# Optimization experiments

Measured on AMD Instinct MI355X. Metric: run time of the kernel, lower is better.

## Reference

```python
import jax, jax.numpy as jnp
import numpy as np

B, S, D, H = 2, 2048, 1024, 16
HD = D // H  # head_dim = 64


def setup_inputs() -> dict:
    key = jax.random.key(0)
    ks = jax.random.split(key, 11)
    s = 0.02  # keep projections well-scaled
    return {
        "Q": jax.random.normal(ks[0], (B, S, D), jnp.float32),
        "K": jax.random.normal(ks[1], (B, S, D), jnp.float32),
        "V": jax.random.normal(ks[2], (B, S, D), jnp.float32),
        "Wq": jax.random.normal(ks[3], (D, D), jnp.float32) * s,
        "bq": jax.random.normal(ks[4], (D,), jnp.float32) * s,
        "Wk": jax.random.normal(ks[5], (D, D), jnp.float32) * s,
        "bk": jax.random.normal(ks[6], (D,), jnp.float32) * s,
        "Wv": jax.random.normal(ks[7], (D, D), jnp.float32) * s,
        "bv": jax.random.normal(ks[8], (D,), jnp.float32) * s,
        "Wo": jax.random.normal(ks[9], (D, D), jnp.float32) * s,
        "bo": jax.random.normal(ks[10], (D,), jnp.float32) * s,
    }


def reference(Q, K, V, Wq, bq, Wk, bk, Wv, bv, Wo, bo):
    b, s, d = Q.shape
    # projections (torch Linear: x @ W.T + b)
    q = (Q @ Wq.T + bq).reshape(b, s, H, HD).transpose(0, 2, 1, 3)  # [B,H,S,HD]
    k = (K @ Wk.T + bk).reshape(b, s, H, HD).transpose(0, 2, 1, 3)
    v = (V @ Wv.T + bv).reshape(b, s, H, HD).transpose(0, 2, 1, 3)
    # scaled dot-product scores: [B,H,S,S]
    scale = 1.0 / jnp.sqrt(jnp.asarray(HD, q.dtype))
    scores = jnp.einsum("bhqd,bhkd->bhqk", q, k) * scale
    # module's explicit max-subtract before softmax
    scores = scores - jnp.max(scores, axis=-1, keepdims=True)
    attn = jax.nn.softmax(scores, axis=-1)
    # dropout p=0.0 (eval) -> identity; renormalize-after-dropout kept verbatim
    attn = attn / jnp.sum(attn, axis=-1, keepdims=True)
    ctx = jnp.einsum("bhqk,bhkd->bhqd", attn, v)  # [B,H,S,HD]
    ctx = ctx.transpose(0, 2, 1, 3).reshape(b, s, d)
    out = ctx @ Wo.T + bo
    return out
```

## Files before the change

kernel.cpp:

```cpp
#include <hip/hip_runtime.h>

#define SS 2048
#define SD 1024
#define SH 16
#define SHD 64
#define MROWS 4096
#define LOG2E 1.44269504088896340736f

typedef __attribute__((ext_vector_type(8))) short short8;
typedef __attribute__((ext_vector_type(4))) short short4v;
typedef __attribute__((ext_vector_type(4))) float floatx4;
typedef __attribute__((ext_vector_type(4))) unsigned short ushort4v;
typedef unsigned short u16;
typedef unsigned int u32;

#define AS1 __attribute__((address_space(1)))
#define AS3 __attribute__((address_space(3)))

__device__ inline u16 f2bf(float v) {
  u32 x = __builtin_bit_cast(u32, v);
  x = x + 0x7fffu + ((x >> 16) & 1u);
  return (u16)(x >> 16);
}

__global__ __launch_bounds__(256) void cast_all(
    const float* __restrict__ q, const float* __restrict__ k,
    const float* __restrict__ v, const float* __restrict__ wq,
    const float* __restrict__ wk, const float* __restrict__ wv,
    const float* __restrict__ wo, u16* __restrict__ out) {
  int i = blockIdx.x * 256 + threadIdx.x;
  const float* src;
  int idx;
  if (i < 3145728) {
    int a = i >> 20;
    src = (a == 0) ? q : ((a == 1) ? k : v);
    idx = i & 1048575;
  } else {
    int j = i - 3145728;
    int a = j >> 18;
    src = (a == 0) ? wq : ((a == 1) ? wk : ((a == 2) ? wv : wo));
    idx = j & 262143;
  }
  float4 f = ((const float4*)src)[idx];
  ushort4v o;
  o[0] = f2bf(f.x); o[1] = f2bf(f.y); o[2] = f2bf(f.z); o[3] = f2bf(f.w);
  ((ushort4v*)out)[i] = o;
}

__global__ __launch_bounds__(256) void gemm_bt(
    const u16* __restrict__ Aall, const u16* __restrict__ Wall,
    const float* __restrict__ b0, const float* __restrict__ b1,
    const float* __restrict__ b2, u16* __restrict__ outb,
    float* __restrict__ outf, int mode, float qscale) {
  __shared__ u16 lds_a[128 * 32];
  __shared__ u16 lds_w[128 * 32];
  int z = blockIdx.z;
  const u16* A = Aall + (size_t)z * (MROWS * (size_t)SD);
  const u16* W = Wall + (size_t)z * (SD * (size_t)SD);
  const float* bias = (z == 0) ? b0 : ((z == 1) ? b1 : b2);
  float scale = (mode == 0 && z == 0) ? qscale : 1.0f;

  int tid = threadIdx.x;
  int lane = tid & 63, wave = tid >> 6;
  int l16 = lane & 15, quad = lane >> 4;
  int wm = (wave >> 1) * 64, wn = (wave & 1) * 64;
  int tm = blockIdx.y * 128, tn = blockIdx.x * 128;

  floatx4 acc[4][4];
  floatx4 zf = {0.f, 0.f, 0.f, 0.f};
#pragma unroll
  for (int r = 0; r < 4; r++)
#pragma unroll
    for (int c = 0; c < 4; c++) acc[r][c] = zf;

  int srow = wave * 16 + (lane >> 2);
  int scol8 = (lane & 3) * 8;
  const u16* pa0 = A + (size_t)(tm + srow) * SD + scol8;
  const u16* pa1 = pa0 + (size_t)64 * SD;
  const u16* pw0 = W + (size_t)(tn + srow) * SD + scol8;
  const u16* pw1 = pw0 + (size_t)64 * SD;
  AS3 u16* la0 = (AS3 u16*)&lds_a[wave * 512];
  AS3 u16* la1 = (AS3 u16*)&lds_a[(wave + 4) * 512];
  AS3 u16* lw0 = (AS3 u16*)&lds_w[wave * 512];
  AS3 u16* lw1 = (AS3 u16*)&lds_w[(wave + 4) * 512];

  for (int k0 = 0; k0 < SD; k0 += 32) {
    __builtin_amdgcn_global_load_lds((const AS1 void*)pa0, (AS3 void*)la0, 16, 0, 0);
    __builtin_amdgcn_global_load_lds((const AS1 void*)pa1, (AS3 void*)la1, 16, 0, 0);
    __builtin_amdgcn_global_load_lds((const AS1 void*)pw0, (AS3 void*)lw0, 16, 0, 0);
    __builtin_amdgcn_global_load_lds((const AS1 void*)pw1, (AS3 void*)lw1, 16, 0, 0);
    pa0 += 32; pa1 += 32; pw0 += 32; pw1 += 32;
    __syncthreads();
    short8 af[4], wf[4];
#pragma unroll
    for (int r = 0; r < 4; r++)
      af[r] = *(short8*)&lds_a[(wm + r * 16 + l16) * 32 + quad * 8];
#pragma unroll
    for (int c = 0; c < 4; c++)
      wf[c] = *(short8*)&lds_w[(wn + c * 16 + l16) * 32 + quad * 8];
#pragma unroll
    for (int r = 0; r < 4; r++)
#pragma unroll
      for (int c = 0; c < 4; c++)
        acc[r][c] = __builtin_amdgcn_mfma_f32_16x16x32_bf16(af[r], wf[c], acc[r][c], 0, 0, 0);
    __syncthreads();
  }

  if (mode == 0) {
    u16* ob = outb + (size_t)z * (MROWS * (size_t)SD);
    if (z < 2) {
#pragma unroll
      for (int r = 0; r < 4; r++) {
#pragma unroll
        for (int c = 0; c < 4; c++) {
          int gn = tn + wn + c * 16 + l16;
          float bv = bias[gn];
          int h = gn >> 6, hd = gn & 63;
#pragma unroll
          for (int g = 0; g < 4; g++) {
            int gm = tm + wm + r * 16 + quad * 4 + g;
            int bb = gm >> 11, ss = gm & 2047;
            float val = (acc[r][c][g] + bv) * scale;
            ob[(size_t)(((bb * SH + h) * SS + ss) * SHD + hd)] = f2bf(val);
          }
        }
      }
    } else {
      int h = (tn + wn) >> 6;
      int bb = (tm + wm) >> 11;
      int kt = ((tm + wm) & 2047) >> 6;
      u16* vbase = ob + (size_t)(bb * SH + h) * (SS * SHD) + (size_t)kt * 4096 +
                   (l16 * 4 + quad) * 8;
#pragma unroll
      for (int c = 0; c < 4; c++) {
        int gn = tn + wn + c * 16 + l16;
        float bv = bias[gn];
#pragma unroll
        for (int rp = 0; rp < 2; rp++) {
          union { u16 u[8]; short8 s; } pk;
#pragma unroll
          for (int g = 0; g < 4; g++) {
            pk.u[g]     = f2bf(acc[2 * rp][c][g] + bv);
            pk.u[4 + g] = f2bf(acc[2 * rp + 1][c][g] + bv);
          }
          *(short8*)&vbase[(c * 2 + rp) * 512] = pk.s;
        }
      }
    }
  } else {
#pragma unroll
    for (int r = 0; r < 4; r++) {
#pragma unroll
      for (int c = 0; c < 4; c++) {
        int gn = tn + wn + c * 16 + l16;
        float bv = bias[gn];
#pragma unroll
        for (int g = 0; g < 4; g++) {
          int gm = tm + wm + r * 16 + quad * 4 + g;
          outf[(size_t)gm * SD + gn] = acc[r][c][g] + bv;
        }
      }
    }
  }
}

__global__ __launch_bounds__(128, 2) void attn(
    const u16* __restrict__ qb, const u16* __restrict__ kb,
    const u16* __restrict__ vfrag, u16* __restrict__ ctxb) {
  int lane = threadIdx.x & 63;
  int wave = threadIdx.x >> 6;
  int l16 = lane & 15, quad = lane >> 4;

  int raw = blockIdx.x;
  int xcd = raw & 7, slot = raw >> 3;
  int bh = xcd + 8 * (slot >> 5);
  int qt = slot & 31;
  int b = bh >> 4, h = bh & 15;
  int base = bh * (SS * SHD);
  int q0 = qt * 64;

  const u16* kp = kb + base + l16 * 64 + quad * 8;
  const u16* vp = vfrag + base + (l16 * 4 + quad) * 8;

  short8 qf[4][2];
#pragma unroll
  for (int t = 0; t < 4; t++)
#pragma unroll
    for (int hh = 0; hh < 2; hh++)
      qf[t][hh] = *(const short8*)&qb[base + (q0 + t * 16 + l16) * SHD + hh * 32 + quad * 8];

  floatx4 zf = {0.f, 0.f, 0.f, 0.f};
  floatx4 acc[4][4], accl[4];
#pragma unroll
  for (int t = 0; t < 4; t++) {
    accl[t] = zf;
#pragma unroll
    for (int c = 0; c < 4; c++) acc[t][c] = zf;
  }
  const short8 ones8 = {0x3F80, 0x3F80, 0x3F80, 0x3F80,
                        0x3F80, 0x3F80, 0x3F80, 0x3F80};

  int ktbase = wave * 16;
  short8 kf[4][2], vf[4][2];
  {
    const u16* p = kp + ktbase * 4096;
#pragma unroll
    for (int ct = 0; ct < 4; ct++)
#pragma unroll
      for (int hh = 0; hh < 2; hh++)
        kf[ct][hh] = *(const short8*)&p[ct * 1024 + hh * 32];
    const u16* pv = vp + ktbase * 4096;
#pragma unroll
    for (int c = 0; c < 4; c++)
#pragma unroll
      for (int c2 = 0; c2 < 2; c2++)
        vf[c][c2] = *(const short8*)&pv[(c * 2 + c2) * 512];
  }

#pragma unroll 1
  for (int i = 0; i < 16; i++) {
    int nt = ktbase + ((i + 1) & 15);
    const u16* kpn = kp + nt * 4096;
    const u16* vpn = vp + nt * 4096;
#pragma unroll
    for (int c2 = 0; c2 < 2; c2++) {
      const int ct0 = 2 * c2, ct1 = 2 * c2 + 1;
      floatx4 se[4], so[4];
#pragma unroll
      for (int t = 0; t < 4; t++) {
        floatx4 zz = zf;
        zz = __builtin_amdgcn_mfma_f32_16x16x32_bf16(kf[ct0][0], qf[t][0], zz, 0, 0, 0);
        zz = __builtin_amdgcn_mfma_f32_16x16x32_bf16(kf[ct0][1], qf[t][1], zz, 0, 0, 0);
        se[t] = zz;
        floatx4 ww = zf;
        ww = __builtin_amdgcn_mfma_f32_16x16x32_bf16(kf[ct1][0], qf[t][0], ww, 0, 0, 0);
        ww = __builtin_amdgcn_mfma_f32_16x16x32_bf16(kf[ct1][1], qf[t][1], ww, 0, 0, 0);
        so[t] = ww;
      }
      kf[ct0][0] = *(const short8*)&kpn[ct0 * 1024];
      kf[ct0][1] = *(const short8*)&kpn[ct0 * 1024 + 32];
      kf[ct1][0] = *(const short8*)&kpn[ct1 * 1024];
      kf[ct1][1] = *(const short8*)&kpn[ct1 * 1024 + 32];
#pragma unroll
      for (int t = 0; t < 4; t++) {
        u32 e0 = __builtin_bit_cast(u32, __builtin_amdgcn_exp2f(se[t][0]));
        u32 e1 = __builtin_bit_cast(u32, __builtin_amdgcn_exp2f(se[t][1]));
        u32 e2 = __builtin_bit_cast(u32, __builtin_amdgcn_exp2f(se[t][2]));
        u32 e3 = __builtin_bit_cast(u32, __builtin_amdgcn_exp2f(se[t][3]));
        u32 o0 = __builtin_bit_cast(u32, __builtin_amdgcn_exp2f(so[t][0]));
        u32 o1 = __builtin_bit_cast(u32, __builtin_amdgcn_exp2f(so[t][1]));
        u32 o2 = __builtin_bit_cast(u32, __builtin_amdgcn_exp2f(so[t][2]));
        u32 o3 = __builtin_bit_cast(u32, __builtin_amdgcn_exp2f(so[t][3]));
        union { u32 u[4]; short8 s; } pa;
        pa.u[0] = __builtin_amdgcn_perm(e1, e0, 0x07060302);
        pa.u[1] = __builtin_amdgcn_perm(e3, e2, 0x07060302);
        pa.u[2] = __builtin_amdgcn_perm(o1, o0, 0x07060302);
        pa.u[3] = __builtin_amdgcn_perm(o3, o2, 0x07060302);
#pragma unroll
        for (int c = 0; c < 4; c++)
          acc[t][c] = __builtin_amdgcn_mfma_f32_16x16x32_bf16(pa.s, vf[c][c2], acc[t][c], 0, 0, 0);
        accl[t] = __builtin_amdgcn_mfma_f32_16x16x32_bf16(pa.s, ones8, accl[t], 0, 0, 0);
      }
#pragma unroll
      for (int c = 0; c < 4; c++)
        vf[c][c2] = *(const short8*)&vpn[(c * 2 + c2) * 512];
    }
  }

  __shared__ floatx4 red[2][64][11];
  int ow = 1 - wave;
#pragma unroll
  for (int t = 0; t < 4; t++) {
    if ((t >> 1) == ow) {
#pragma unroll
      for (int c = 0; c < 4; c++) red[ow][lane][(t & 1) * 5 + c] = acc[t][c];
      red[ow][lane][(t & 1) * 5 + 4] = accl[t];
    }
  }
  __syncthreads();
#pragma unroll
  for (int t = 0; t < 4; t++) {
    if ((t >> 1) == wave) {
#pragma unroll
      for (int c = 0; c < 4; c++) acc[t][c] += red[wave][lane][(t & 1) * 5 + c];
      accl[t] += red[wave][lane][(t & 1) * 5 + 4];
    }
  }

#pragma unroll
  for (int t = 0; t < 4; t++) {
    if ((t >> 1) == wave) {
#pragma unroll
      for (int g = 0; g < 4; g++) {
        float invg = 1.0f / accl[t][g];
        int qrow = q0 + t * 16 + quad * 4 + g;
#pragma unroll
        for (int c = 0; c < 4; c++) {
          int hd = c * 16 + l16;
          ctxb[(size_t)((b * SS + qrow) * SD + h * SHD + hd)] = f2bf(acc[t][c][g] * invg);
        }
      }
    }
  }
}

extern "C" void kernel_launch(void* const* d_in, const int* in_sizes, int n_in,
                              void* d_out, int out_size, void* d_ws, size_t ws_size,
                              hipStream_t stream) {
  const float* Q  = (const float*)d_in[0];
  const float* Kp = (const float*)d_in[1];
  const float* Vp = (const float*)d_in[2];
  const float* Wq = (const float*)d_in[3];
  const float* bq = (const float*)d_in[4];
  const float* Wk = (const float*)d_in[5];
  const float* bk = (const float*)d_in[6];
  const float* Wv = (const float*)d_in[7];
  const float* bv = (const float*)d_in[8];
  const float* Wo = (const float*)d_in[9];
  const float* bo = (const float*)d_in[10];

  u16* xb   = (u16*)d_ws;
  u16* wb   = xb + (size_t)3 * 4194304;
  u16* qkvb = wb + (size_t)4 * 1048576;
  u16* ctxb = qkvb + (size_t)3 * 4194304;
  float* out = (float*)d_out;

  cast_all<<<dim3(16384), dim3(256), 0, stream>>>(Q, Kp, Vp, Wq, Wk, Wv, Wo, xb);

  const float qscale = 0.125f * LOG2E;
  gemm_bt<<<dim3(8, 32, 3), dim3(256), 0, stream>>>(
      xb, wb, bq, bk, bv, qkvb, (float*)nullptr, 0, qscale);

  attn<<<dim3(1024), dim3(128), 0, stream>>>(
      qkvb, qkvb + (size_t)4194304, qkvb + (size_t)2 * 4194304, ctxb);

  gemm_bt<<<dim3(8, 32, 1), dim3(256), 0, stream>>>(
      ctxb, wb + (size_t)3 * 1048576, bo, bo, bo,
      (u16*)nullptr, out, 1, 1.0f);
}
```

Measured before the change: 242.6 us.

## Use swizzled 64-wide K tiles in GEMM and fragment-packed Q/K layout

The projection GEMM now stages 64-wide K slices per iteration in an XOR-swizzled LDS layout, halving the number of barriers and reducing bank conflicts. It also sets an occupancy hint of three blocks per SM. For Q and K, the epilogue stages the tile through LDS and writes MFMA-fragment-ordered chunks, so each lane does one contiguous 16-byte load in the attention kernel instead of strided row loads. The cost is twice the LDS per block and an extra LDS round trip plus a barrier in the epilogue.

```diff
diff --git a/kernel.cpp b/kernel.cpp
--- a/kernel.cpp
+++ b/kernel.cpp
@@ -47,13 +47,14 @@
   ((ushort4v*)out)[i] = o;
 }
 
-__global__ __launch_bounds__(256) void gemm_bt(
+__global__ __launch_bounds__(256, 3) void gemm_bt(
     const u16* __restrict__ Aall, const u16* __restrict__ Wall,
     const float* __restrict__ b0, const float* __restrict__ b1,
     const float* __restrict__ b2, u16* __restrict__ outb,
     float* __restrict__ outf, int mode, float qscale) {
-  __shared__ u16 lds_a[128 * 32];
-  __shared__ u16 lds_w[128 * 32];
+  __shared__ u16 smem[16384];
+  u16* lds_a = smem;
+  u16* lds_w = smem + 8192;
   int z = blockIdx.z;
   const u16* A = Aall + (size_t)z * (MROWS * (size_t)SD);
   const u16* W = Wall + (size_t)z * (SD * (size_t)SD);
@@ -73,57 +74,81 @@
 #pragma unroll
     for (int c = 0; c < 4; c++) acc[r][c] = zf;
 
-  int srow = wave * 16 + (lane >> 2);
-  int scol8 = (lane & 3) * 8;
-  const u16* pa0 = A + (size_t)(tm + srow) * SD + scol8;
-  const u16* pa1 = pa0 + (size_t)64 * SD;
-  const u16* pw0 = W + (size_t)(tn + srow) * SD + scol8;
-  const u16* pw1 = pw0 + (size_t)64 * SD;
-  AS3 u16* la0 = (AS3 u16*)&lds_a[wave * 512];
-  AS3 u16* la1 = (AS3 u16*)&lds_a[(wave + 4) * 512];
-  AS3 u16* lw0 = (AS3 u16*)&lds_w[wave * 512];
-  AS3 u16* lw1 = (AS3 u16*)&lds_w[(wave + 4) * 512];
-
-  for (int k0 = 0; k0 < SD; k0 += 32) {
-    __builtin_amdgcn_global_load_lds((const AS1 void*)pa0, (AS3 void*)la0, 16, 0, 0);
-    __builtin_amdgcn_global_load_lds((const AS1 void*)pa1, (AS3 void*)la1, 16, 0, 0);
-    __builtin_amdgcn_global_load_lds((const AS1 void*)pw0, (AS3 void*)lw0, 16, 0, 0);
-    __builtin_amdgcn_global_load_lds((const AS1 void*)pw1, (AS3 void*)lw1, 16, 0, 0);
-    pa0 += 32; pa1 += 32; pw0 += 32; pw1 += 32;
+  const u16* pa[4];
+  const u16* pw[4];
+#pragma unroll
+  for (int q = 0; q < 4; q++) {
+    int srow = q * 32 + wave * 8 + (lane >> 3);
+    int scol = (((lane & 7) ^ ((lane >> 3) & 7)) << 3);
+    pa[q] = A + (size_t)(tm + srow) * SD + scol;
+    pw[q] = W + (size_t)(tn + srow) * SD + scol;
+  }
+
+  for (int k0 = 0; k0 < SD; k0 += 64) {
+#pragma unroll
+    for (int q = 0; q < 4; q++) {
+      __builtin_amdgcn_global_load_lds((const AS1 void*)pa[q],
+          (AS3 void*)(AS3 u16*)&lds_a[(q * 32 + wave * 8) * 64], 16, 0, 0);
+      __builtin_amdgcn_global_load_lds((const AS1 void*)pw[q],
+          (AS3 void*)(AS3 u16*)&lds_w[(q * 32 + wave * 8) * 64], 16, 0, 0);
+      pa[q] += 64; pw[q] += 64;
+    }
     __syncthreads();
-    short8 af[4], wf[4];
+    short8 af[4][2], wf[4][2];
 #pragma unroll
     for (int r = 0; r < 4; r++)
-      af[r] = *(short8*)&lds_a[(wm + r * 16 + l16) * 32 + quad * 8];
+#pragma unroll
+      for (int kk = 0; kk < 2; kk++)
+        af[r][kk] = *(short8*)&lds_a[(wm + r * 16 + l16) * 64 +
+                                     (((kk * 4 + quad) ^ (l16 & 7)) << 3)];
 #pragma unroll
     for (int c = 0; c < 4; c++)
-      wf[c] = *(short8*)&lds_w[(wn + c * 16 + l16) * 32 + quad * 8];
+#pragma unroll
+      for (int kk = 0; kk < 2; kk++)
+        wf[c][kk] = *(short8*)&lds_w[(wn + c * 16 + l16) * 64 +
+                                     (((kk * 4 + quad) ^ (l16 & 7)) << 3)];
 #pragma unroll
     for (int r = 0; r < 4; r++)
 #pragma unroll
-      for (int c = 0; c < 4; c++)
-        acc[r][c] = __builtin_amdgcn_mfma_f32_16x16x32_bf16(af[r], wf[c], acc[r][c], 0, 0, 0);
+      for (int c = 0; c < 4; c++) {
+        acc[r][c] = __builtin_amdgcn_mfma_f32_16x16x32_bf16(af[r][0], wf[c][0], acc[r][c], 0, 0, 0);
+        acc[r][c] = __builtin_amdgcn_mfma_f32_16x16x32_bf16(af[r][1], wf[c][1], acc[r][c], 0, 0, 0);
+      }
     __syncthreads();
   }
 
   if (mode == 0) {
     u16* ob = outb + (size_t)z * (MROWS * (size_t)SD);
     if (z < 2) {
+      u16* LT = smem;
 #pragma unroll
       for (int r = 0; r < 4; r++) {
 #pragma unroll
         for (int c = 0; c < 4; c++) {
-          int gn = tn + wn + c * 16 + l16;
-          float bv = bias[gn];
-          int h = gn >> 6, hd = gn & 63;
+          int feat = wn + c * 16 + l16;
+          float bv = bias[tn + feat];
 #pragma unroll
           for (int g = 0; g < 4; g++) {
-            int gm = tm + wm + r * 16 + quad * 4 + g;
-            int bb = gm >> 11, ss = gm & 2047;
+            int key = wm + r * 16 + quad * 4 + g;
             float val = (acc[r][c][g] + bv) * scale;
-            ob[(size_t)(((bb * SH + h) * SS + ss) * SHD + hd)] = f2bf(val);
+            LT[key * 128 + ((((feat >> 3) ^ (key & 7)) << 3) | (feat & 7))] = f2bf(val);
           }
         }
+      }
+      __syncthreads();
+      int bb = tm >> 11;
+      int kt0 = (tm & 2047) >> 6;
+#pragma unroll
+      for (int i = 0; i < 8; i++) {
+        int id = wave * 8 + i;
+        int kt_rel = id >> 4, hrel = (id >> 3) & 1, ct = (id >> 1) & 3, hh = id & 1;
+        int key = kt_rel * 64 + ct * 16 + l16;
+        int chunk = hrel * 8 + hh * 4 + quad;
+        short8 vv = *(short8*)&LT[key * 128 + ((chunk ^ (l16 & 7)) << 3)];
+        int h = (tn >> 6) + hrel;
+        u16* dst = ob + (size_t)(bb * SH + h) * (SS * SHD) +
+                   ((kt0 + kt_rel) * 8 + ct * 2 + hh) * 512 + lane * 8;
+        *(short8*)dst = vv;
       }
     } else {
       int h = (tn + wn) >> 6;
@@ -179,7 +204,7 @@
   int base = bh * (SS * SHD);
   int q0 = qt * 64;
 
-  const u16* kp = kb + base + l16 * 64 + quad * 8;
+  const u16* kp = kb + base + lane * 8;
   const u16* vp = vfrag + base + (l16 * 4 + quad) * 8;
 
   short8 qf[4][2];
@@ -187,7 +212,7 @@
   for (int t = 0; t < 4; t++)
 #pragma unroll
     for (int hh = 0; hh < 2; hh++)
-      qf[t][hh] = *(const short8*)&qb[base + (q0 + t * 16 + l16) * SHD + hh * 32 + quad * 8];
+      qf[t][hh] = *(const short8*)&qb[base + (qt * 8 + t * 2 + hh) * 512 + lane * 8];
 
   floatx4 zf = {0.f, 0.f, 0.f, 0.f};
   floatx4 acc[4][4], accl[4];
@@ -208,7 +233,7 @@
     for (int ct = 0; ct < 4; ct++)
 #pragma unroll
       for (int hh = 0; hh < 2; hh++)
-        kf[ct][hh] = *(const short8*)&p[ct * 1024 + hh * 32];
+        kf[ct][hh] = *(const short8*)&p[(ct * 2 + hh) * 512];
     const u16* pv = vp + ktbase * 4096;
 #pragma unroll
     for (int c = 0; c < 4; c++)
@@ -237,10 +262,10 @@
         ww = __builtin_amdgcn_mfma_f32_16x16x32_bf16(kf[ct1][1], qf[t][1], ww, 0, 0, 0);
         so[t] = ww;
       }
-      kf[ct0][0] = *(const short8*)&kpn[ct0 * 1024];
-      kf[ct0][1] = *(const short8*)&kpn[ct0 * 1024 + 32];
-      kf[ct1][0] = *(const short8*)&kpn[ct1 * 1024];
-      kf[ct1][1] = *(const short8*)&kpn[ct1 * 1024 + 32];
+      kf[ct0][0] = *(const short8*)&kpn[(ct0 * 2 + 0) * 512];
+      kf[ct0][1] = *(const short8*)&kpn[(ct0 * 2 + 1) * 512];
+      kf[ct1][0] = *(const short8*)&kpn[(ct1 * 2 + 0) * 512];
+      kf[ct1][1] = *(const short8*)&kpn[(ct1 * 2 + 1) * 512];
 #pragma unroll
       for (int t = 0; t < 4; t++) {
         u32 e0 = __builtin_bit_cast(u32, __builtin_amdgcn_exp2f(se[t][0]));
```

Result: faster. 206.7 us (-14.8%).
